# Optimization experiments

Measured on AMD Instinct MI355X. Metric: run time of the kernel, lower is better.

Reference implementation:

```python
import jax, jax.numpy as jnp
import numpy as np

B, R, NB, T = 32, 96, 5, 2048
FEAT_DIM = 64
SPARSITY = 0.2


def _per_band(X, community, W1, b1, W2, b2):
    # X: [R, T] wavelet coeffs for one (batch, band) slice
    n, t = X.shape
    f32 = X.dtype
    # --- functional connectivity (cosine of centered signals == Pearson corr) ---
    Xc = X - X.mean(axis=1, keepdims=True)
    norm = jnp.linalg.norm(Xc, axis=1, keepdims=True)
    norm = jnp.where(norm == 0, 1.0, norm)
    C = (Xc @ Xc.T) / (norm * norm.T)
    C = jnp.nan_to_num(C, nan=0.0)
    C = C * (1.0 - jnp.eye(n, dtype=f32))  # zero diagonal
    # --- quantile sparsification over strict lower triangle ---
    ti, tj = np.tril_indices(n, -1)
    thr = jnp.quantile(jnp.abs(C[ti, tj]), 1.0 - SPARSITY)
    A = C * (jnp.abs(C) >= thr).astype(f32)  # graph_type == 'weighted'
    # --- node features (5-dim, averaged over regions) ---
    mean_f = X.mean(axis=1)
    std_f = jnp.std(X, axis=1, ddof=1)  # torch.std is unbiased
    energy_f = (X ** 2).sum(axis=1)
    maxamp_f = jnp.abs(X).max(axis=1)
    ps = jnp.abs(jnp.fft.fft(X, axis=1)) ** 2
    ps = ps[:, : t // 2]
    s = ps.sum(axis=1, keepdims=True)
    s = jnp.where(s == 0, 1.0, s)
    p = ps / s
    ent_f = -(p * jnp.log(p + 1e-10)).sum(axis=1)
    node5 = jnp.stack([mean_f, std_f, energy_f, maxamp_f, ent_f], axis=1).mean(axis=0)
    # --- graph properties (6-dim) on binarized adjacency ---
    Bm = (A != 0).astype(f32)
    ne = Bm.sum() / 2.0
    density = ne / (n * (n - 1) / 2.0)
    deg = Bm.sum(axis=1)
    avg_deg = deg.mean()
    A2 = Bm @ Bm
    tri = (A2 * Bm).sum() / 6.0
    poss = (deg * (deg - 1.0)).sum() / 2.0
    clus = jnp.where(poss > 0, tri / jnp.where(poss > 0, poss, 1.0), 0.0)
    # global efficiency: safe reciprocal (zero where A+I == 0; original would emit inf)
    denom = Bm + jnp.eye(n, dtype=f32)
    eff = jnp.where(denom > 0, 1.0 / jnp.where(denom > 0, denom, 1.0), 0.0).sum() / (n * (n - 1))
    # approximate modularity with fixed 2-community assignment (deterministic)
    m2 = 2.0 * ne
    m2_safe = jnp.where(m2 > 0, m2, 1.0)
    same = (community[:, None] == community[None, :]) & (~jnp.eye(n, dtype=bool))
    expected = jnp.outer(deg, deg) / m2_safe
    mod = jnp.where(m2 > 0, (same * (Bm - expected)).sum() / m2_safe, 0.0)
    props = jnp.stack([ne, density, avg_deg, clus, eff, mod])
    feat11 = jnp.concatenate([node5, props])  # [11]
    # --- feature encoder MLP (dropout is identity at inference) ---
    h = jnp.maximum(feat11 @ W1.T + b1, 0.0)
    return A, h @ W2.T + b2


def _forward(wavelet_coeffs, frequency_bands, community, W1, b1, W2, b2):
    b, r, nb, t = wavelet_coeffs.shape
    Xs = wavelet_coeffs.transpose(0, 2, 1, 3).reshape(b * nb, r, t)  # [B*NB, R, T]
    A, F = jax.vmap(_per_band, in_axes=(0, None, None, None, None, None))(
        Xs, community, W1, b1, W2, b2)
    return A.reshape(b, nb, r, r), F.reshape(b, nb, -1)


def setup_inputs() -> dict:
    key = jax.random.key(0)
    k0, k1, k2, k3, k4 = jax.random.split(key, 5)
    wavelet_coeffs = jax.random.normal(k0, (B, R, NB, T), dtype=jnp.float32)
    frequency_bands = jax.random.uniform(k1, (NB, 2), dtype=jnp.float32)
    community = jax.random.randint(k2, (R,), 0, 2)
    W1 = jax.random.normal(k3, (32, 11), dtype=jnp.float32) * 0.3
    b1 = jnp.zeros((32,), jnp.float32)
    W2 = jax.random.normal(k4, (FEAT_DIM, 32), dtype=jnp.float32) * 0.18
    b2 = jnp.zeros((FEAT_DIM,), jnp.float32)
    return {"wavelet_coeffs": wavelet_coeffs, "frequency_bands": frequency_bands,
            "community": community, "W1": W1, "b1": b1, "W2": W2, "b2": b2}


def reference(wavelet_coeffs, frequency_bands, community, W1, b1, W2, b2):
    return _forward(wavelet_coeffs, frequency_bands, community, W1, b1, W2, b2)
```

## Files before the change

### kernel.cpp

```cpp
#include <hip/hip_runtime.h>
#include <hip/hip_bf16.h>
#include <math.h>
#include <float.h>

#ifndef M_PI
#define M_PI 3.14159265358979323846
#endif

#define NBANDS 160
#define RR 96
#define TT 2048
#define NTRIL 4560
#define A_ELEMS ((size_t)NBANDS * RR * RR)
#define NBIN 16384
#define MAXCAND 512

#define PHI(L) ((L) ^ (((L) >> 5) & 31))

typedef float  f32x4  __attribute__((ext_vector_type(4)));
typedef __bf16 bf16x8 __attribute__((ext_vector_type(8)));
typedef __bf16 bf16x4 __attribute__((ext_vector_type(4)));

__device__ inline double blockReduceSum(double v, double* sred) {
    for (int off = 32; off > 0; off >>= 1) v += __shfl_down(v, off, 64);
    int lane = threadIdx.x & 63, wid = threadIdx.x >> 6;
    if (lane == 0) sred[wid] = v;
    __syncthreads();
    int nw = (blockDim.x + 63) >> 6;
    if (threadIdx.x == 0) {
        double r = sred[0];
        for (int i = 1; i < nw; i++) r += sred[i];
        sred[0] = r;
    }
    __syncthreads();
    double r = sred[0];
    __syncthreads();
    return r;
}

__device__ inline void blockReduceSum4(double v0, double v1, double v2, double v3,
                                       double* sred, double out[4]) {
    for (int off = 32; off > 0; off >>= 1) {
        v0 += __shfl_down(v0, off, 64);
        v1 += __shfl_down(v1, off, 64);
        v2 += __shfl_down(v2, off, 64);
        v3 += __shfl_down(v3, off, 64);
    }
    int lane = threadIdx.x & 63, wid = threadIdx.x >> 6;
    if (lane == 0) {
        sred[wid * 4 + 0] = v0; sred[wid * 4 + 1] = v1;
        sred[wid * 4 + 2] = v2; sred[wid * 4 + 3] = v3;
    }
    __syncthreads();
    if (threadIdx.x < 4) {
        double r = sred[threadIdx.x] + sred[4 + threadIdx.x]
                 + sred[8 + threadIdx.x] + sred[12 + threadIdx.x];
        sred[16 + threadIdx.x] = r;
    }
    __syncthreads();
    out[0] = sred[16]; out[1] = sred[17]; out[2] = sred[18]; out[3] = sred[19];
    __syncthreads();
}

__device__ inline void blockReduceSum2(double v0, double v1,
                                       double* sred, double out[2]) {
    for (int off = 32; off > 0; off >>= 1) {
        v0 += __shfl_down(v0, off, 64);
        v1 += __shfl_down(v1, off, 64);
    }
    int lane = threadIdx.x & 63, wid = threadIdx.x >> 6;
    if (lane == 0) { sred[wid * 2 + 0] = v0; sred[wid * 2 + 1] = v1; }
    __syncthreads();
    if (threadIdx.x < 2) {
        double r = sred[threadIdx.x] + sred[2 + threadIdx.x]
                 + sred[4 + threadIdx.x] + sred[6 + threadIdx.x];
        sred[8 + threadIdx.x] = r;
    }
    __syncthreads();
    out[0] = sred[8]; out[1] = sred[9];
    __syncthreads();
}

__device__ inline void blockReduceMax2(double v0, double v1,
                                       double* sred, double out[2]) {
    for (int off = 32; off > 0; off >>= 1) {
        v0 = fmax(v0, __shfl_down(v0, off, 64));
        v1 = fmax(v1, __shfl_down(v1, off, 64));
    }
    int lane = threadIdx.x & 63, wid = threadIdx.x >> 6;
    if (lane == 0) { sred[wid * 2 + 0] = v0; sred[wid * 2 + 1] = v1; }
    __syncthreads();
    if (threadIdx.x < 2) {
        double r = fmax(fmax(sred[threadIdx.x], sred[2 + threadIdx.x]),
                        fmax(sred[4 + threadIdx.x], sred[6 + threadIdx.x]));
        sred[8 + threadIdx.x] = r;
    }
    __syncthreads();
    out[0] = sred[8]; out[1] = sred[9];
    __syncthreads();
}

__global__ void twiddle_kernel(float* tw) {
    int k = blockIdx.x * blockDim.x + threadIdx.x;
    if (k < 1024) {
        double ang = -2.0 * M_PI * (double)k / 2048.0;
        tw[2 * k]     = (float)cos(ang);
        tw[2 * k + 1] = (float)sin(ang);
    }
}

#define BFLY(r1, r2, WR, WI) do { \
    float _wr = (WR), _wi = (WI); \
    float _tr = _wr * yr[r2] - _wi * yi[r2]; \
    float _ti = _wr * yi[r2] + _wi * yr[r2]; \
    yr[r2] = yr[r1] - _tr; yi[r2] = yi[r1] - _ti; \
    yr[r1] += _tr; yi[r1] += _ti; } while (0)

__global__ __launch_bounds__(256) void rowstat_fft_kernel(
    const float* __restrict__ wc, const float* __restrict__ tw,
    double* __restrict__ rowstats)
{
    __shared__ float re[TT];
    __shared__ float im[TT];
    __shared__ double sred[24];
    __shared__ float bcast[4];

    int t = threadIdx.x;
    int g0 = blockIdx.x * 2;
    int g1 = g0 + 1;

    int band = g0 / RR, r0 = g0 % RR;
    int b = band / 5, nb = band % 5;
    size_t base0 = ((size_t)(b * RR + r0) * 5 + nb) * TT;
    size_t base1 = base0 + (size_t)5 * TT;

    float s0 = 0.f, s1 = 0.f, q0 = 0.f, q1 = 0.f, m0 = 0.f, m1 = 0.f;
#pragma unroll
    for (int c = 0; c < 8; c++) {
        int i = t + c * 256;
        float af = wc[base0 + i];
        float bf = wc[base1 + i];
        int P = PHI(i);
        re[P] = af; im[P] = bf;
        s0 += af; s1 += bf;
        q0 = fmaf(af, af, q0); q1 = fmaf(bf, bf, q1);
        m0 = fmaxf(m0, fabsf(af)); m1 = fmaxf(m1, fabsf(bf));
    }
    __syncthreads();

    double S4[4], M2[2];
    blockReduceSum4((double)s0, (double)s1, (double)q0, (double)q1, sred, S4);
    blockReduceMax2((double)m0, (double)m1, sred, M2);
    double SUM0 = S4[0], SUM1 = S4[1], SQ0 = S4[2], SQ1 = S4[3];
    double MX0 = M2[0], MX1 = M2[1];

    float yr[8], yi[8];

#pragma unroll
    for (int j = 0; j < 8; j++) {
        int p = 8 * t + j;
        int L = (int)(__brev((unsigned)p) >> 21);
        int P = PHI(L);
        yr[j] = re[P]; yi[j] = im[P];
    }

    const float RC = 0.70710678f;
    BFLY(0, 1, 1.0f, 0.0f); BFLY(2, 3, 1.0f, 0.0f);
    BFLY(4, 5, 1.0f, 0.0f); BFLY(6, 7, 1.0f, 0.0f);
    BFLY(0, 2, 1.0f, 0.0f); BFLY(1, 3, 0.0f, -1.0f);
    BFLY(4, 6, 1.0f, 0.0f); BFLY(5, 7, 0.0f, -1.0f);
    BFLY(0, 4, 1.0f, 0.0f); BFLY(1, 5, RC, -RC);
    BFLY(2, 6, 0.0f, -1.0f); BFLY(3, 7, -RC, -RC);

    __syncthreads();
#pragma unroll
    for (int j = 0; j < 8; j++) {
        int P = PHI(8 * t + j);
        re[P] = yr[j]; im[P] = yi[j];
    }
    __syncthreads();
    int oo = t & 7;
    int bb64 = 4 * ((t >> 3) & 7) + (t >> 6);
#pragma unroll
    for (int k = 0; k < 8; k++) {
        int P = PHI(64 * bb64 + 8 * k + oo);
        yr[k] = re[P]; yi[k] = im[P];
    }

    {
        int k0 = oo << 7;
        float w0r = tw[2 * k0], w0i = tw[2 * k0 + 1];
        BFLY(0, 1, w0r, w0i); BFLY(2, 3, w0r, w0i);
        BFLY(4, 5, w0r, w0i); BFLY(6, 7, w0r, w0i);
        int ka = oo << 6, kb = (oo + 8) << 6;
        float war = tw[2 * ka], wai = tw[2 * ka + 1];
        float wbr = tw[2 * kb], wbi = tw[2 * kb + 1];
        BFLY(0, 2, war, wai); BFLY(1, 3, wbr, wbi);
        BFLY(4, 6, war, wai); BFLY(5, 7, wbr, wbi);
        int kc0 = oo << 5, kc1 = (oo + 8) << 5, kc2 = (oo + 16) << 5, kc3 = (oo + 24) << 5;
        BFLY(0, 4, tw[2 * kc0], tw[2 * kc0 + 1]);
        BFLY(1, 5, tw[2 * kc1], tw[2 * kc1 + 1]);
        BFLY(2, 6, tw[2 * kc2], tw[2 * kc2 + 1]);
        BFLY(3, 7, tw[2 * kc3], tw[2 * kc3 + 1]);
    }

    __syncthreads();
#pragma unroll
    for (int k = 0; k < 8; k++) {
        int P = PHI(64 * bb64 + 8 * k + oo);
        re[P] = yr[k]; im[P] = yi[k];
    }
    __syncthreads();
    int O3 = t & 63, Wq = t >> 6;
#pragma unroll
    for (int s = 0; s < 2; s++) {
        int B3 = Wq + 4 * s;
#pragma unroll
        for (int k = 0; k < 4; k++) {
            int P = PHI(256 * B3 + 64 * k + O3);
            yr[4 * s + k] = re[P]; yi[4 * s + k] = im[P];
        }
    }

    {
        int kt = O3 << 4;
        float w0r = tw[2 * kt], w0i = tw[2 * kt + 1];
        int ka = O3 << 3, kb = (O3 + 64) << 3;
        float war = tw[2 * ka], wai = tw[2 * ka + 1];
        float wbr = tw[2 * kb], wbi = tw[2 * kb + 1];
        BFLY(0, 1, w0r, w0i); BFLY(2, 3, w0r, w0i);
        BFLY(4, 5, w0r, w0i); BFLY(6, 7, w0r, w0i);
        BFLY(0, 2, war, wai); BFLY(1, 3, wbr, wbi);
        BFLY(4, 6, war, wai); BFLY(5, 7, wbr, wbi);
    }

    __syncthreads();
#pragma unroll
    for (int s = 0; s < 2; s++) {
        int B3 = Wq + 4 * s;
#pragma unroll
        for (int k = 0; k < 4; k++) {
            int P = PHI(256 * B3 + 64 * k + O3);
            re[P] = yr[4 * s + k]; im[P] = yi[4 * s + k];
        }
    }
    __syncthreads();
#pragma unroll
    for (int k = 0; k < 8; k++) {
        int P = PHI(256 * k + t);
        yr[k] = re[P]; yi[k] = im[P];
    }

    {
        int k9 = t << 2;
        float w0r = tw[2 * k9], w0i = tw[2 * k9 + 1];
        BFLY(0, 1, w0r, w0i); BFLY(2, 3, w0r, w0i);
        BFLY(4, 5, w0r, w0i); BFLY(6, 7, w0r, w0i);
        int ka = t << 1, kb = (t + 256) << 1;
        float war = tw[2 * ka], wai = tw[2 * ka + 1];
        float wbr = tw[2 * kb], wbi = tw[2 * kb + 1];
        BFLY(0, 2, war, wai); BFLY(1, 3, wbr, wbi);
        BFLY(4, 6, war, wai); BFLY(5, 7, wbr, wbi);
        BFLY(0, 4, tw[2 * t], tw[2 * t + 1]);
        BFLY(1, 5, tw[2 * (t + 256)], tw[2 * (t + 256) + 1]);
        BFLY(2, 6, tw[2 * (t + 512)], tw[2 * (t + 512) + 1]);
        BFLY(3, 7, tw[2 * (t + 768)], tw[2 * (t + 768) + 1]);
    }

    __syncthreads();
#pragma unroll
    for (int k = 0; k < 8; k++) {
        int P = PHI(256 * k + t);
        re[P] = yr[k]; im[P] = yi[k];
    }
    __syncthreads();

    float psa[8], psb[8];
#pragma unroll
    for (int k = 0; k < 8; k++) {
        int q = (2048 - t - 256 * k) & 2047;
        int P = PHI(q);
        float prr = re[P], pii = im[P];
        float sr = yr[k] + prr, di = yi[k] - pii;
        float si = yi[k] + pii, dr = yr[k] - prr;
        psa[k] = 0.25f * (sr * sr + di * di);
        psb[k] = 0.25f * (si * si + dr * dr);
    }

    float la = 0.f, lb = 0.f;
#pragma unroll
    for (int k = 0; k < 8; k++) { la += psa[k]; lb += psb[k]; }
    double SS[2];
    blockReduceSum2((double)la, (double)lb, sred, SS);
    double SAall = SS[0], SBall = SS[1];
    if (t == 0) {
        bcast[0] = psa[0]; bcast[1] = psa[4];
        bcast[2] = psb[0]; bcast[3] = psb[4];
    }
    __syncthreads();
    double Sa = 0.5 * (SAall + (double)bcast[0] - (double)bcast[1]);
    double Sb = 0.5 * (SBall + (double)bcast[2] - (double)bcast[3]);
    if (Sa == 0.0) Sa = 1.0;
    if (Sb == 0.0) Sb = 1.0;
    float invSa = (float)(1.0 / Sa), invSb = (float)(1.0 / Sb);

    float ea = 0.f, eb = 0.f;
#pragma unroll
    for (int k = 0; k < 8; k++) {
        float pa = psa[k] * invSa;
        float pb = psb[k] * invSb;
        ea += pa * __logf(pa + 1e-10f);
        eb += pb * __logf(pb + 1e-10f);
    }
    double EE[2];
    blockReduceSum2((double)ea, (double)eb, sred, EE);
    double EAall = EE[0], EBall = EE[1];

    if (t == 0) {
        float pa0 = psa[0] * invSa, pa4 = psa[4] * invSa;
        float pb0 = psb[0] * invSb, pb4 = psb[4] * invSb;
        double TA = 0.5 * (EAall + (double)(pa0 * __logf(pa0 + 1e-10f))
                                 - (double)(pa4 * __logf(pa4 + 1e-10f)));
        double TB = 0.5 * (EBall + (double)(pb0 * __logf(pb0 + 1e-10f))
                                 - (double)(pb4 * __logf(pb4 + 1e-10f)));
        double mean0 = SUM0 / (double)TT;
        double mean1 = SUM1 / (double)TT;
        double nsq0 = SQ0 - (double)TT * mean0 * mean0; if (nsq0 < 0) nsq0 = 0;
        double nsq1 = SQ1 - (double)TT * mean1 * mean1; if (nsq1 < 0) nsq1 = 0;
        double* w0 = rowstats + (size_t)g0 * 6;
        double* w1 = rowstats + (size_t)g1 * 6;
        double n0 = sqrt(nsq0), n1 = sqrt(nsq1);
        w0[0] = mean0; w0[1] = (n0 == 0.0 ? 1.0 : n0); w0[2] = sqrt(nsq0 / 2047.0);
        w0[3] = SQ0;   w0[4] = MX0;                    w0[5] = -TA;
        w1[0] = mean1; w1[1] = (n1 == 0.0 ? 1.0 : n1); w1[2] = sqrt(nsq1 / 2047.0);
        w1[3] = SQ1;   w1[4] = MX1;                    w1[5] = -TB;
    }
}

__global__ void zero_kernel(float4* __restrict__ p, int n4) {
    int i = blockIdx.x * blockDim.x + threadIdx.x;
    if (i < n4) p[i] = make_float4(0.f, 0.f, 0.f, 0.f);
}

#define KS 8
#define CHUNK 256
#define BKS 64
#define GPITCH 72
template <bool USE_PART>
__global__ __launch_bounds__(384) void gram_mfma_kernel(
    const float* __restrict__ wc, float* __restrict__ G)
{
    __shared__ __attribute__((aligned(16))) __bf16 sh_hi[RR][GPITCH];
    __shared__ __attribute__((aligned(16))) __bf16 sh_lo[RR][GPITCH];

    int bid = blockIdx.x;
    int band = bid / KS, chunk = bid % KS;
    int b = band / 5, nb = band % 5;
    size_t bandbase = ((size_t)b * RR * 5 + nb) * TT + (size_t)chunk * CHUNK;

    int t = threadIdx.x;
    int wave = t >> 6, lane = t & 63;
    int m16 = lane & 15, quad = lane >> 4;
    int arow = wave * 16 + m16;

    f32x4 acc[6];
#pragma unroll
    for (int ct = 0; ct < 6; ct++) acc[ct] = (f32x4){0.f, 0.f, 0.f, 0.f};

    for (int stage = 0; stage < CHUNK / BKS; stage++) {
        int k0 = stage * BKS;
#pragma unroll
        for (int i = 0; i < 4; i++) {
            int gid = t + i * 384;
            int row = gid >> 4, c4 = gid & 15;
            float4 v = *(const float4*)(wc + bandbase + (size_t)row * (5 * TT) + k0 + c4 * 4);
            __bf16 h0 = (__bf16)v.x, h1 = (__bf16)v.y, h2 = (__bf16)v.z, h3 = (__bf16)v.w;
            __bf16 l0 = (__bf16)(v.x - (float)h0);
            __bf16 l1 = (__bf16)(v.y - (float)h1);
            __bf16 l2 = (__bf16)(v.z - (float)h2);
            __bf16 l3 = (__bf16)(v.w - (float)h3);
            *(bf16x4*)&sh_hi[row][c4 * 4] = (bf16x4){h0, h1, h2, h3};
            *(bf16x4*)&sh_lo[row][c4 * 4] = (bf16x4){l0, l1, l2, l3};
        }
        __syncthreads();
#pragma unroll
        for (int ks = 0; ks < BKS / 32; ks++) {
            int ko = ks * 32 + quad * 8;
            bf16x8 ah = *(const bf16x8*)&sh_hi[arow][ko];
            bf16x8 al = *(const bf16x8*)&sh_lo[arow][ko];
#pragma unroll
            for (int ct = 0; ct < 6; ct++) {
                int brow = ct * 16 + m16;
                bf16x8 bh = *(const bf16x8*)&sh_hi[brow][ko];
                bf16x8 bl = *(const bf16x8*)&sh_lo[brow][ko];
                acc[ct] = __builtin_amdgcn_mfma_f32_16x16x32_bf16(ah, bh, acc[ct], 0, 0, 0);
                acc[ct] = __builtin_amdgcn_mfma_f32_16x16x32_bf16(ah, bl, acc[ct], 0, 0, 0);
                acc[ct] = __builtin_amdgcn_mfma_f32_16x16x32_bf16(al, bh, acc[ct], 0, 0, 0);
            }
        }
        __syncthreads();
    }

    if (USE_PART) {
        float* Gp = G + (size_t)bid * (RR * RR);
#pragma unroll
        for (int ct = 0; ct < 6; ct++) {
#pragma unroll
            for (int r = 0; r < 4; r++) {
                int grow = wave * 16 + quad * 4 + r;
                int gcol = ct * 16 + m16;
                Gp[grow * RR + gcol] = acc[ct][r];
            }
        }
    } else {
        float* Gb = G + (size_t)band * (RR * RR);
#pragma unroll
        for (int ct = 0; ct < 6; ct++) {
#pragma unroll
            for (int r = 0; r < 4; r++) {
                int grow = wave * 16 + quad * 4 + r;
                int gcol = ct * 16 + m16;
                atomicAdd(&Gb[grow * RR + gcol], acc[ct][r]);
            }
        }
    }
}

template <bool USE_PART>
__global__ __launch_bounds__(256) void normalize_kernel(
    float* __restrict__ G, const float* __restrict__ Gpart,
    const double* __restrict__ rowstats)
{
    int e = blockIdx.x * 256 + threadIdx.x;
    if (e >= (int)(NBANDS * RR * RR)) return;
    int band = e / (RR * RR);
    int rem = e % (RR * RR);
    int i = rem / RR, j = rem % RR;
    double g;
    if (USE_PART) {
        const float* p = Gpart + (size_t)band * KS * (RR * RR) + rem;
        float acc = 0.f;
#pragma unroll
        for (int c = 0; c < KS; c++) acc += p[(size_t)c * (RR * RR)];
        g = (double)acc;
    } else {
        g = (double)G[e];
    }
    const double* rsi = rowstats + (size_t)(band * RR + i) * 6;
    const double* rsj = rowstats + (size_t)(band * RR + j) * 6;
    double c = (g - (double)TT * rsi[0] * rsj[0]) / (rsi[1] * rsj[1]);
    if (i == j) c = 0.0;
    G[e] = (float)c;
}

__global__ __launch_bounds__(256) void quantile_kernel(
    const float* __restrict__ C, double* __restrict__ thr)
{
    __shared__ int hist[NBIN];
    __shared__ int chunk[256];
    __shared__ float cand[MAXCAND];
    __shared__ int ctrl[4];

    int band = blockIdx.x, t = threadIdx.x;
    const float* Cb = C + (size_t)band * (RR * RR);

    for (int i = t; i < NBIN; i += 256) hist[i] = 0;
    if (t == 0) ctrl[3] = 0;
    __syncthreads();

    for (int idx = t; idx < RR * RR; idx += 256) {
        int i = idx / RR, j = idx % RR;
        if (j < i) {
            float val = fabsf(Cb[idx]);
            int bin = (int)(val * (float)NBIN);
            bin = bin > (NBIN - 1) ? (NBIN - 1) : bin;
            atomicAdd(&hist[bin], 1);
        }
    }
    __syncthreads();

    int cs = 0;
    for (int i = 0; i < 64; i++) cs += hist[t * 64 + i];
    chunk[t] = cs;
    __syncthreads();

    if (t == 0) {
        int r0 = 3647, r1 = 3648;
        int cum = 0, c0 = 0;
        while (c0 < 256 && cum + chunk[c0] <= r0) { cum += chunk[c0]; c0++; }
        int bin = c0 * 64, cb = cum;
        while (cb + hist[bin] <= r0) { cb += hist[bin]; bin++; }
        int B0 = bin, cumB0 = cb;
        int bin1 = bin, cb1 = cb;
        while (cb1 + hist[bin1] <= r1) { cb1 += hist[bin1]; bin1++; }
        ctrl[0] = B0; ctrl[1] = bin1; ctrl[2] = cumB0;
    }
    __syncthreads();

    int B0 = ctrl[0], B1 = ctrl[1];
    for (int idx = t; idx < RR * RR; idx += 256) {
        int i = idx / RR, j = idx % RR;
        if (j < i) {
            float val = fabsf(Cb[idx]);
            int bin = (int)(val * (float)NBIN);
            bin = bin > (NBIN - 1) ? (NBIN - 1) : bin;
            if (bin >= B0 && bin <= B1) {
                int k = atomicAdd(&ctrl[3], 1);
                if (k < MAXCAND) cand[k] = val;
            }
        }
    }
    __syncthreads();

    if (t == 0) {
        int n = ctrl[3]; if (n > MAXCAND) n = MAXCAND;
        for (int i = 1; i < n; i++) {
            float key = cand[i]; int j = i - 1;
            while (j >= 0 && cand[j] > key) { cand[j + 1] = cand[j]; j--; }
            cand[j + 1] = key;
        }
        int r0 = 3647 - ctrl[2];
        int r1 = 3648 - ctrl[2];
        double v0 = (double)cand[r0], v1 = (double)cand[r1];
        thr[band] = v0 + 0.2 * (v1 - v0);
    }
}

__global__ __launch_bounds__(256) void graph_feat_kernel(
    const double* __restrict__ thrA,
    const double* __restrict__ rowstats, const int* __restrict__ community,
    const float* __restrict__ W1, const float* __restrict__ b1,
    const float* __restrict__ W2, const float* __restrict__ b2,
    float* __restrict__ A_out, float* __restrict__ F_out)
{
    __shared__ unsigned char Bm[RR][RR];
    __shared__ unsigned long long msk[RR][2];
    __shared__ int deg[RR];
    __shared__ double sred[8];
    __shared__ double feat[11];
    __shared__ double h[32];

    int band = blockIdx.x, t = threadIdx.x;
    double thr = thrA[band];
    float* Ab = A_out + (size_t)band * (RR * RR);

    for (int idx = t; idx < RR * RR; idx += 256) {
        float c = Ab[idx];
        bool keep = ((double)fabsf(c) >= thr);
        Bm[idx / RR][idx % RR] = (keep && c != 0.0f) ? 1 : 0;
        Ab[idx] = keep ? c : 0.0f;
    }
    __syncthreads();

    if (t < RR) {
        unsigned long long m0 = 0, m1 = 0; int d = 0;
        for (int j = 0; j < RR; j++) {
            if (Bm[t][j]) { d++; if (j < 64) m0 |= (1ull << j); else m1 |= (1ull << (j - 64)); }
        }
        msk[t][0] = m0; msk[t][1] = m1; deg[t] = d;
    }
    __syncthreads();

    double triord = 0, ein = 0, expin = 0;
    for (int idx = t; idx < RR * RR; idx += 256) {
        int i = idx / RR, j = idx % RR;
        if (Bm[i][j])
            triord += (double)(__popcll(msk[i][0] & msk[j][0]) +
                               __popcll(msk[i][1] & msk[j][1]));
        if (i != j && community[i] == community[j]) {
            ein += (double)Bm[i][j];
            expin += (double)deg[i] * (double)deg[j];
        }
    }
    double TRI   = blockReduceSum(triord, sred);
    double EIN   = blockReduceSum(ein, sred);
    double EXPIN = blockReduceSum(expin, sred);
    double dv = (t < RR) ? (double)deg[t] : 0.0;
    double DEGS = blockReduceSum(dv, sred);
    double POSS2 = blockReduceSum((t < RR) ? dv * (dv - 1.0) : 0.0, sred);

    const double* rs = rowstats + (size_t)band * RR * 6;
    double N0 = blockReduceSum((t < RR) ? rs[t * 6 + 0] : 0.0, sred);
    double N1 = blockReduceSum((t < RR) ? rs[t * 6 + 2] : 0.0, sred);
    double N2 = blockReduceSum((t < RR) ? rs[t * 6 + 3] : 0.0, sred);
    double N3 = blockReduceSum((t < RR) ? rs[t * 6 + 4] : 0.0, sred);
    double N4 = blockReduceSum((t < RR) ? rs[t * 6 + 5] : 0.0, sred);

    if (t == 0) {
        double ne = 0.5 * DEGS;
        feat[0] = N0 / (double)RR;
        feat[1] = N1 / (double)RR;
        feat[2] = N2 / (double)RR;
        feat[3] = N3 / (double)RR;
        feat[4] = N4 / (double)RR;
        feat[5] = ne;
        feat[6] = ne / (double)NTRIL;
        feat[7] = DEGS / (double)RR;
        double tri = TRI / 6.0, poss = POSS2 * 0.5;
        feat[8] = (poss > 0.0) ? tri / poss : 0.0;
        feat[9] = ((double)RR + DEGS) / ((double)RR * (double)(RR - 1));
        double m2 = DEGS;
        feat[10] = (m2 > 0.0) ? (EIN - EXPIN / m2) / m2 : 0.0;
    }
    __syncthreads();

    if (t < 32) {
        double a = (double)b1[t];
        for (int k = 0; k < 11; k++) a += (double)W1[t * 11 + k] * feat[k];
        h[t] = (a > 0.0) ? a : 0.0;
    }
    __syncthreads();
    if (t < 64) {
        double a = (double)b2[t];
        for (int j = 0; j < 32; j++) a += (double)W2[t * 32 + j] * h[j];
        F_out[(size_t)band * 64 + t] = (float)a;
    }
}

extern "C" void kernel_launch(void* const* d_in, const int* in_sizes, int n_in,
                              void* d_out, int out_size, void* d_ws, size_t ws_size,
                              hipStream_t stream) {
    const float* wc        = (const float*)d_in[0];
    const int*   community = (const int*)d_in[2];
    const float* W1        = (const float*)d_in[3];
    const float* b1        = (const float*)d_in[4];
    const float* W2        = (const float*)d_in[5];
    const float* b2        = (const float*)d_in[6];

    float* A_out = (float*)d_out;
    float* F_out = A_out + A_ELEMS;

    char* ws = (char*)d_ws;
    float*  tw       = (float*)ws;
    double* rowstats = (double*)(ws + 8192);
    double* thr      = (double*)(ws + 745472);
    const size_t PART_OFF   = 747520;
    const size_t PART_BYTES = (size_t)NBANDS * KS * RR * RR * sizeof(float);
    float* Gpart = (float*)(ws + PART_OFF);
    bool use_part = (ws_size >= PART_OFF + PART_BYTES);

    hipLaunchKernelGGL(twiddle_kernel, dim3(4), dim3(256), 0, stream, tw);
    hipLaunchKernelGGL(rowstat_fft_kernel, dim3(NBANDS * RR / 2), dim3(256), 0, stream,
                       wc, tw, rowstats);
    if (use_part) {
        hipLaunchKernelGGL(HIP_KERNEL_NAME(gram_mfma_kernel<true>),
                           dim3(NBANDS * KS), dim3(384), 0, stream, wc, Gpart);
        hipLaunchKernelGGL(HIP_KERNEL_NAME(normalize_kernel<true>),
                           dim3((int)((NBANDS * RR * RR + 255) / 256)), dim3(256), 0, stream,
                           A_out, Gpart, rowstats);
    } else {
        int n4 = (int)(A_ELEMS / 4);
        hipLaunchKernelGGL(zero_kernel, dim3((n4 + 255) / 256), dim3(256), 0, stream,
                           (float4*)A_out, n4);
        hipLaunchKernelGGL(HIP_KERNEL_NAME(gram_mfma_kernel<false>),
                           dim3(NBANDS * KS), dim3(384), 0, stream, wc, A_out);
        hipLaunchKernelGGL(HIP_KERNEL_NAME(normalize_kernel<false>),
                           dim3((int)((NBANDS * RR * RR + 255) / 256)), dim3(256), 0, stream,
                           A_out, A_out, rowstats);
    }
    hipLaunchKernelGGL(quantile_kernel, dim3(NBANDS), dim3(256), 0, stream, A_out, thr);
    hipLaunchKernelGGL(graph_feat_kernel, dim3(NBANDS), dim3(256), 0, stream,
                       thr, rowstats, community, W1, b1, W2, b2, A_out, F_out);
}
```

Before: 323.0 us.

## Fuse gram, normalize, quantile and graph features into one per-band kernel

Replaces the split-K gram kernel plus the normalize, quantile and graph-feature kernels with one kernel per band. That kernel computes the full 2048-long gram product with register prefetch, normalizes into shared memory, builds the histogram, finds the quantile threshold, and derives masks with wave ballots. This removes the partial-sum and correlation-matrix round trips through global memory and several launches. The trade-off is that parallelism for the gram product drops from 1280 blocks to 160, each looping over the whole time axis with heavy shared memory use. Twiddle loads are also vectorized as float2, and the histogram shrinks to 8192 bins.

```diff
diff --git a/kernel.cpp b/kernel.cpp
--- a/kernel.cpp
+++ b/kernel.cpp
@@ -12,31 +12,17 @@
 #define TT 2048
 #define NTRIL 4560
 #define A_ELEMS ((size_t)NBANDS * RR * RR)
-#define NBIN 16384
+#define NBIN 8192
 #define MAXCAND 512
+#define BKS 64
+#define GPITCH 72
+#define FBLK 384
 
 #define PHI(L) ((L) ^ (((L) >> 5) & 31))
 
 typedef float  f32x4  __attribute__((ext_vector_type(4)));
 typedef __bf16 bf16x8 __attribute__((ext_vector_type(8)));
 typedef __bf16 bf16x4 __attribute__((ext_vector_type(4)));
-
-__device__ inline double blockReduceSum(double v, double* sred) {
-    for (int off = 32; off > 0; off >>= 1) v += __shfl_down(v, off, 64);
-    int lane = threadIdx.x & 63, wid = threadIdx.x >> 6;
-    if (lane == 0) sred[wid] = v;
-    __syncthreads();
-    int nw = (blockDim.x + 63) >> 6;
-    if (threadIdx.x == 0) {
-        double r = sred[0];
-        for (int i = 1; i < nw; i++) r += sred[i];
-        sred[0] = r;
-    }
-    __syncthreads();
-    double r = sred[0];
-    __syncthreads();
-    return r;
-}
 
 __device__ inline void blockReduceSum4(double v0, double v1, double v2, double v3,
                                        double* sred, double out[4]) {
@@ -47,18 +33,20 @@
         v3 += __shfl_down(v3, off, 64);
     }
     int lane = threadIdx.x & 63, wid = threadIdx.x >> 6;
+    int nw = blockDim.x >> 6;
     if (lane == 0) {
         sred[wid * 4 + 0] = v0; sred[wid * 4 + 1] = v1;
         sred[wid * 4 + 2] = v2; sred[wid * 4 + 3] = v3;
     }
     __syncthreads();
     if (threadIdx.x < 4) {
-        double r = sred[threadIdx.x] + sred[4 + threadIdx.x]
-                 + sred[8 + threadIdx.x] + sred[12 + threadIdx.x];
-        sred[16 + threadIdx.x] = r;
-    }
-    __syncthreads();
-    out[0] = sred[16]; out[1] = sred[17]; out[2] = sred[18]; out[3] = sred[19];
+        double r = sred[threadIdx.x];
+        for (int w = 1; w < nw; w++) r += sred[w * 4 + threadIdx.x];
+        sred[nw * 4 + threadIdx.x] = r;
+    }
+    __syncthreads();
+    out[0] = sred[nw * 4 + 0]; out[1] = sred[nw * 4 + 1];
+    out[2] = sred[nw * 4 + 2]; out[3] = sred[nw * 4 + 3];
     __syncthreads();
 }
 
@@ -69,15 +57,16 @@
         v1 += __shfl_down(v1, off, 64);
     }
     int lane = threadIdx.x & 63, wid = threadIdx.x >> 6;
+    int nw = blockDim.x >> 6;
     if (lane == 0) { sred[wid * 2 + 0] = v0; sred[wid * 2 + 1] = v1; }
     __syncthreads();
     if (threadIdx.x < 2) {
-        double r = sred[threadIdx.x] + sred[2 + threadIdx.x]
-                 + sred[4 + threadIdx.x] + sred[6 + threadIdx.x];
-        sred[8 + threadIdx.x] = r;
-    }
-    __syncthreads();
-    out[0] = sred[8]; out[1] = sred[9];
+        double r = sred[threadIdx.x];
+        for (int w = 1; w < nw; w++) r += sred[w * 2 + threadIdx.x];
+        sred[nw * 2 + threadIdx.x] = r;
+    }
+    __syncthreads();
+    out[0] = sred[nw * 2 + 0]; out[1] = sred[nw * 2 + 1];
     __syncthreads();
 }
 
@@ -88,15 +77,16 @@
         v1 = fmax(v1, __shfl_down(v1, off, 64));
     }
     int lane = threadIdx.x & 63, wid = threadIdx.x >> 6;
+    int nw = blockDim.x >> 6;
     if (lane == 0) { sred[wid * 2 + 0] = v0; sred[wid * 2 + 1] = v1; }
     __syncthreads();
     if (threadIdx.x < 2) {
-        double r = fmax(fmax(sred[threadIdx.x], sred[2 + threadIdx.x]),
-                        fmax(sred[4 + threadIdx.x], sred[6 + threadIdx.x]));
-        sred[8 + threadIdx.x] = r;
-    }
-    __syncthreads();
-    out[0] = sred[8]; out[1] = sred[9];
+        double r = sred[threadIdx.x];
+        for (int w = 1; w < nw; w++) r = fmax(r, sred[w * 2 + threadIdx.x]);
+        sred[nw * 2 + threadIdx.x] = r;
+    }
+    __syncthreads();
+    out[0] = sred[nw * 2 + 0]; out[1] = sred[nw * 2 + 1];
     __syncthreads();
 }
 
@@ -122,7 +112,7 @@
 {
     __shared__ float re[TT];
     __shared__ float im[TT];
-    __shared__ double sred[24];
+    __shared__ double sred[32];
     __shared__ float bcast[4];
 
     int t = threadIdx.x;
@@ -133,6 +123,7 @@
     int b = band / 5, nb = band % 5;
     size_t base0 = ((size_t)(b * RR + r0) * 5 + nb) * TT;
     size_t base1 = base0 + (size_t)5 * TT;
+    const float2* twv = (const float2*)tw;
 
     float s0 = 0.f, s1 = 0.f, q0 = 0.f, q1 = 0.f, m0 = 0.f, m1 = 0.f;
 #pragma unroll
@@ -188,20 +179,19 @@
     }
 
     {
-        int k0 = oo << 7;
-        float w0r = tw[2 * k0], w0i = tw[2 * k0 + 1];
-        BFLY(0, 1, w0r, w0i); BFLY(2, 3, w0r, w0i);
-        BFLY(4, 5, w0r, w0i); BFLY(6, 7, w0r, w0i);
-        int ka = oo << 6, kb = (oo + 8) << 6;
-        float war = tw[2 * ka], wai = tw[2 * ka + 1];
-        float wbr = tw[2 * kb], wbi = tw[2 * kb + 1];
-        BFLY(0, 2, war, wai); BFLY(1, 3, wbr, wbi);
-        BFLY(4, 6, war, wai); BFLY(5, 7, wbr, wbi);
-        int kc0 = oo << 5, kc1 = (oo + 8) << 5, kc2 = (oo + 16) << 5, kc3 = (oo + 24) << 5;
-        BFLY(0, 4, tw[2 * kc0], tw[2 * kc0 + 1]);
-        BFLY(1, 5, tw[2 * kc1], tw[2 * kc1 + 1]);
-        BFLY(2, 6, tw[2 * kc2], tw[2 * kc2 + 1]);
-        BFLY(3, 7, tw[2 * kc3], tw[2 * kc3 + 1]);
+        float2 w0 = twv[oo << 7];
+        BFLY(0, 1, w0.x, w0.y); BFLY(2, 3, w0.x, w0.y);
+        BFLY(4, 5, w0.x, w0.y); BFLY(6, 7, w0.x, w0.y);
+        float2 wa = twv[oo << 6];
+        float2 wb = twv[(oo + 8) << 6];
+        BFLY(0, 2, wa.x, wa.y); BFLY(1, 3, wb.x, wb.y);
+        BFLY(4, 6, wa.x, wa.y); BFLY(5, 7, wb.x, wb.y);
+        float2 wc0 = twv[oo << 5], wc1 = twv[(oo + 8) << 5];
+        float2 wc2 = twv[(oo + 16) << 5], wc3 = twv[(oo + 24) << 5];
+        BFLY(0, 4, wc0.x, wc0.y);
+        BFLY(1, 5, wc1.x, wc1.y);
+        BFLY(2, 6, wc2.x, wc2.y);
+        BFLY(3, 7, wc3.x, wc3.y);
     }
 
     __syncthreads();
@@ -223,15 +213,13 @@
     }
 
     {
-        int kt = O3 << 4;
-        float w0r = tw[2 * kt], w0i = tw[2 * kt + 1];
-        int ka = O3 << 3, kb = (O3 + 64) << 3;
-        float war = tw[2 * ka], wai = tw[2 * ka + 1];
-        float wbr = tw[2 * kb], wbi = tw[2 * kb + 1];
-        BFLY(0, 1, w0r, w0i); BFLY(2, 3, w0r, w0i);
-        BFLY(4, 5, w0r, w0i); BFLY(6, 7, w0r, w0i);
-        BFLY(0, 2, war, wai); BFLY(1, 3, wbr, wbi);
-        BFLY(4, 6, war, wai); BFLY(5, 7, wbr, wbi);
+        float2 w0 = twv[O3 << 4];
+        float2 wa = twv[O3 << 3];
+        float2 wb = twv[(O3 + 64) << 3];
+        BFLY(0, 1, w0.x, w0.y); BFLY(2, 3, w0.x, w0.y);
+        BFLY(4, 5, w0.x, w0.y); BFLY(6, 7, w0.x, w0.y);
+        BFLY(0, 2, wa.x, wa.y); BFLY(1, 3, wb.x, wb.y);
+        BFLY(4, 6, wa.x, wa.y); BFLY(5, 7, wb.x, wb.y);
     }
 
     __syncthreads();
@@ -252,19 +240,19 @@
     }
 
     {
-        int k9 = t << 2;
-        float w0r = tw[2 * k9], w0i = tw[2 * k9 + 1];
-        BFLY(0, 1, w0r, w0i); BFLY(2, 3, w0r, w0i);
-        BFLY(4, 5, w0r, w0i); BFLY(6, 7, w0r, w0i);
-        int ka = t << 1, kb = (t + 256) << 1;
-        float war = tw[2 * ka], wai = tw[2 * ka + 1];
-        float wbr = tw[2 * kb], wbi = tw[2 * kb + 1];
-        BFLY(0, 2, war, wai); BFLY(1, 3, wbr, wbi);
-        BFLY(4, 6, war, wai); BFLY(5, 7, wbr, wbi);
-        BFLY(0, 4, tw[2 * t], tw[2 * t + 1]);
-        BFLY(1, 5, tw[2 * (t + 256)], tw[2 * (t + 256) + 1]);
-        BFLY(2, 6, tw[2 * (t + 512)], tw[2 * (t + 512) + 1]);
-        BFLY(3, 7, tw[2 * (t + 768)], tw[2 * (t + 768) + 1]);
+        float2 w0 = twv[t << 2];
+        float2 wa = twv[t << 1];
+        float2 wb = twv[(t + 256) << 1];
+        BFLY(0, 1, w0.x, w0.y); BFLY(2, 3, w0.x, w0.y);
+        BFLY(4, 5, w0.x, w0.y); BFLY(6, 7, w0.x, w0.y);
+        BFLY(0, 2, wa.x, wa.y); BFLY(1, 3, wb.x, wb.y);
+        BFLY(4, 6, wa.x, wa.y); BFLY(5, 7, wb.x, wb.y);
+        float2 wf0 = twv[t], wf1 = twv[t + 256];
+        float2 wf2 = twv[t + 512], wf3 = twv[t + 768];
+        BFLY(0, 4, wf0.x, wf0.y);
+        BFLY(1, 5, wf1.x, wf1.y);
+        BFLY(2, 6, wf2.x, wf2.y);
+        BFLY(3, 7, wf3.x, wf3.y);
     }
 
     __syncthreads();
@@ -337,52 +325,83 @@
     }
 }
 
-__global__ void zero_kernel(float4* __restrict__ p, int n4) {
-    int i = blockIdx.x * blockDim.x + threadIdx.x;
-    if (i < n4) p[i] = make_float4(0.f, 0.f, 0.f, 0.f);
-}
-
-#define KS 8
-#define CHUNK 256
-#define BKS 64
-#define GPITCH 72
-template <bool USE_PART>
-__global__ __launch_bounds__(384) void gram_mfma_kernel(
-    const float* __restrict__ wc, float* __restrict__ G)
+#define CVW(v, row, c4) do { \
+    __bf16 _h0 = (__bf16)v.x, _h1 = (__bf16)v.y, _h2 = (__bf16)v.z, _h3 = (__bf16)v.w; \
+    __bf16 _l0 = (__bf16)(v.x - (float)_h0), _l1 = (__bf16)(v.y - (float)_h1); \
+    __bf16 _l2 = (__bf16)(v.z - (float)_h2), _l3 = (__bf16)(v.w - (float)_h3); \
+    *(bf16x4*)&sh_hi[row][(c4) * 4] = (bf16x4){_h0, _h1, _h2, _h3}; \
+    *(bf16x4*)&sh_lo[row][(c4) * 4] = (bf16x4){_l0, _l1, _l2, _l3}; } while (0)
+
+__global__ __launch_bounds__(FBLK) void fused_gram_finalize_kernel(
+    const float* __restrict__ wc, const double* __restrict__ rowstats,
+    const int* __restrict__ community,
+    const float* __restrict__ W1, const float* __restrict__ b1,
+    const float* __restrict__ W2, const float* __restrict__ b2,
+    float* __restrict__ A_out, float* __restrict__ F_out)
 {
     __shared__ __attribute__((aligned(16))) __bf16 sh_hi[RR][GPITCH];
     __shared__ __attribute__((aligned(16))) __bf16 sh_lo[RR][GPITCH];
-
-    int bid = blockIdx.x;
-    int band = bid / KS, chunk = bid % KS;
+    __shared__ float Cs[RR][RR];
+    __shared__ int hist[NBIN];
+    __shared__ int chunkv[256];
+    __shared__ float cand[MAXCAND];
+    __shared__ int ctrl[4];
+    __shared__ double mean_s[RR], inv_s[RR];
+    __shared__ int comm_s[RR];
+    __shared__ unsigned long long msk[RR][2];
+    __shared__ int deg[RR];
+    __shared__ double sred[32];
+    __shared__ double feat[11];
+    __shared__ double hmlp[32];
+    __shared__ double thr_s;
+
+    int band = blockIdx.x, t = threadIdx.x;
     int b = band / 5, nb = band % 5;
-    size_t bandbase = ((size_t)b * RR * 5 + nb) * TT + (size_t)chunk * CHUNK;
-
-    int t = threadIdx.x;
+    size_t bandbase = ((size_t)b * RR * 5 + nb) * TT;
+    const double* rsb = rowstats + (size_t)band * RR * 6;
+
+    if (t < RR) {
+        mean_s[t] = rsb[t * 6 + 0];
+        inv_s[t]  = 1.0 / rsb[t * 6 + 1];
+        comm_s[t] = community[t];
+    }
+    for (int i = t; i < NBIN; i += FBLK) hist[i] = 0;
+    if (t == 0) ctrl[3] = 0;
+
     int wave = t >> 6, lane = t & 63;
     int m16 = lane & 15, quad = lane >> 4;
     int arow = wave * 16 + m16;
 
+    int gid0 = t, gid1 = t + 384, gid2 = t + 768, gid3 = t + 1152;
+    int row0 = gid0 >> 4, c40 = gid0 & 15;
+    int row1 = gid1 >> 4, c41 = gid1 & 15;
+    int row2 = gid2 >> 4, c42 = gid2 & 15;
+    int row3 = gid3 >> 4, c43 = gid3 & 15;
+    const float* p0 = wc + bandbase + (size_t)row0 * (5 * TT) + c40 * 4;
+    const float* p1 = wc + bandbase + (size_t)row1 * (5 * TT) + c41 * 4;
+    const float* p2 = wc + bandbase + (size_t)row2 * (5 * TT) + c42 * 4;
+    const float* p3 = wc + bandbase + (size_t)row3 * (5 * TT) + c43 * 4;
+
     f32x4 acc[6];
 #pragma unroll
     for (int ct = 0; ct < 6; ct++) acc[ct] = (f32x4){0.f, 0.f, 0.f, 0.f};
 
-    for (int stage = 0; stage < CHUNK / BKS; stage++) {
-        int k0 = stage * BKS;
-#pragma unroll
-        for (int i = 0; i < 4; i++) {
-            int gid = t + i * 384;
-            int row = gid >> 4, c4 = gid & 15;
-            float4 v = *(const float4*)(wc + bandbase + (size_t)row * (5 * TT) + k0 + c4 * 4);
-            __bf16 h0 = (__bf16)v.x, h1 = (__bf16)v.y, h2 = (__bf16)v.z, h3 = (__bf16)v.w;
-            __bf16 l0 = (__bf16)(v.x - (float)h0);
-            __bf16 l1 = (__bf16)(v.y - (float)h1);
-            __bf16 l2 = (__bf16)(v.z - (float)h2);
-            __bf16 l3 = (__bf16)(v.w - (float)h3);
-            *(bf16x4*)&sh_hi[row][c4 * 4] = (bf16x4){h0, h1, h2, h3};
-            *(bf16x4*)&sh_lo[row][c4 * 4] = (bf16x4){l0, l1, l2, l3};
-        }
+    float4 pr0 = *(const float4*)(p0);
+    float4 pr1 = *(const float4*)(p1);
+    float4 pr2 = *(const float4*)(p2);
+    float4 pr3 = *(const float4*)(p3);
+
+    for (int st = 0; st < TT / BKS; st++) {
+        CVW(pr0, row0, c40); CVW(pr1, row1, c41);
+        CVW(pr2, row2, c42); CVW(pr3, row3, c43);
         __syncthreads();
+        if (st + 1 < TT / BKS) {
+            int k0 = (st + 1) * BKS;
+            pr0 = *(const float4*)(p0 + k0);
+            pr1 = *(const float4*)(p1 + k0);
+            pr2 = *(const float4*)(p2 + k0);
+            pr3 = *(const float4*)(p3 + k0);
+        }
 #pragma unroll
         for (int ks = 0; ks < BKS / 32; ks++) {
             int ko = ks * 32 + quad * 8;
@@ -401,94 +420,40 @@
         __syncthreads();
     }
 
-    if (USE_PART) {
-        float* Gp = G + (size_t)bid * (RR * RR);
-#pragma unroll
-        for (int ct = 0; ct < 6; ct++) {
-#pragma unroll
-            for (int r = 0; r < 4; r++) {
-                int grow = wave * 16 + quad * 4 + r;
-                int gcol = ct * 16 + m16;
-                Gp[grow * RR + gcol] = acc[ct][r];
+#pragma unroll
+    for (int ct = 0; ct < 6; ct++) {
+#pragma unroll
+        for (int r = 0; r < 4; r++) {
+            int grow = wave * 16 + quad * 4 + r;
+            int gcol = ct * 16 + m16;
+            double cd = ((double)acc[ct][r]
+                         - (double)TT * mean_s[grow] * mean_s[gcol])
+                        * (inv_s[grow] * inv_s[gcol]);
+            if (grow == gcol) cd = 0.0;
+            float cf = (float)cd;
+            Cs[grow][gcol] = cf;
+            if (gcol < grow) {
+                float val = fabsf(cf);
+                int bin = (int)(val * (float)NBIN);
+                bin = bin > (NBIN - 1) ? (NBIN - 1) : bin;
+                atomicAdd(&hist[bin], 1);
             }
         }
-    } else {
-        float* Gb = G + (size_t)band * (RR * RR);
-#pragma unroll
-        for (int ct = 0; ct < 6; ct++) {
-#pragma unroll
-            for (int r = 0; r < 4; r++) {
-                int grow = wave * 16 + quad * 4 + r;
-                int gcol = ct * 16 + m16;
-                atomicAdd(&Gb[grow * RR + gcol], acc[ct][r]);
-            }
-        }
-    }
-}
-
-template <bool USE_PART>
-__global__ __launch_bounds__(256) void normalize_kernel(
-    float* __restrict__ G, const float* __restrict__ Gpart,
-    const double* __restrict__ rowstats)
-{
-    int e = blockIdx.x * 256 + threadIdx.x;
-    if (e >= (int)(NBANDS * RR * RR)) return;
-    int band = e / (RR * RR);
-    int rem = e % (RR * RR);
-    int i = rem / RR, j = rem % RR;
-    double g;
-    if (USE_PART) {
-        const float* p = Gpart + (size_t)band * KS * (RR * RR) + rem;
-        float acc = 0.f;
-#pragma unroll
-        for (int c = 0; c < KS; c++) acc += p[(size_t)c * (RR * RR)];
-        g = (double)acc;
-    } else {
-        g = (double)G[e];
-    }
-    const double* rsi = rowstats + (size_t)(band * RR + i) * 6;
-    const double* rsj = rowstats + (size_t)(band * RR + j) * 6;
-    double c = (g - (double)TT * rsi[0] * rsj[0]) / (rsi[1] * rsj[1]);
-    if (i == j) c = 0.0;
-    G[e] = (float)c;
-}
-
-__global__ __launch_bounds__(256) void quantile_kernel(
-    const float* __restrict__ C, double* __restrict__ thr)
-{
-    __shared__ int hist[NBIN];
-    __shared__ int chunk[256];
-    __shared__ float cand[MAXCAND];
-    __shared__ int ctrl[4];
-
-    int band = blockIdx.x, t = threadIdx.x;
-    const float* Cb = C + (size_t)band * (RR * RR);
-
-    for (int i = t; i < NBIN; i += 256) hist[i] = 0;
-    if (t == 0) ctrl[3] = 0;
-    __syncthreads();
-
-    for (int idx = t; idx < RR * RR; idx += 256) {
-        int i = idx / RR, j = idx % RR;
-        if (j < i) {
-            float val = fabsf(Cb[idx]);
-            int bin = (int)(val * (float)NBIN);
-            bin = bin > (NBIN - 1) ? (NBIN - 1) : bin;
-            atomicAdd(&hist[bin], 1);
-        }
-    }
-    __syncthreads();
-
-    int cs = 0;
-    for (int i = 0; i < 64; i++) cs += hist[t * 64 + i];
-    chunk[t] = cs;
+    }
+    __syncthreads();
+
+    if (t < 256) {
+        int cs = 0;
+        for (int i = 0; i < NBIN / 256; i++) cs += hist[t * (NBIN / 256) + i];
+        chunkv[t] = cs;
+    }
     __syncthreads();
 
     if (t == 0) {
         int r0 = 3647, r1 = 3648;
         int cum = 0, c0 = 0;
-        while (c0 < 256 && cum + chunk[c0] <= r0) { cum += chunk[c0]; c0++; }
-        int bin = c0 * 64, cb = cum;
+        while (c0 < 256 && cum + chunkv[c0] <= r0) { cum += chunkv[c0]; c0++; }
+        int bin = c0 * (NBIN / 256), cb = cum;
         while (cb + hist[bin] <= r0) { cb += hist[bin]; bin++; }
         int B0 = bin, cumB0 = cb;
         int bin1 = bin, cb1 = cb;
@@ -498,10 +463,10 @@
     __syncthreads();
 
     int B0 = ctrl[0], B1 = ctrl[1];
-    for (int idx = t; idx < RR * RR; idx += 256) {
+    for (int idx = t; idx < RR * RR; idx += FBLK) {
         int i = idx / RR, j = idx % RR;
         if (j < i) {
-            float val = fabsf(Cb[idx]);
+            float val = fabsf(Cs[i][j]);
             int bin = (int)(val * (float)NBIN);
             bin = bin > (NBIN - 1) ? (NBIN - 1) : bin;
             if (bin >= B0 && bin <= B1) {
@@ -522,69 +487,57 @@
         int r0 = 3647 - ctrl[2];
         int r1 = 3648 - ctrl[2];
         double v0 = (double)cand[r0], v1 = (double)cand[r1];
-        thr[band] = v0 + 0.2 * (v1 - v0);
-    }
-}
-
-__global__ __launch_bounds__(256) void graph_feat_kernel(
-    const double* __restrict__ thrA,
-    const double* __restrict__ rowstats, const int* __restrict__ community,
-    const float* __restrict__ W1, const float* __restrict__ b1,
-    const float* __restrict__ W2, const float* __restrict__ b2,
-    float* __restrict__ A_out, float* __restrict__ F_out)
-{
-    __shared__ unsigned char Bm[RR][RR];
-    __shared__ unsigned long long msk[RR][2];
-    __shared__ int deg[RR];
-    __shared__ double sred[8];
-    __shared__ double feat[11];
-    __shared__ double h[32];
-
-    int band = blockIdx.x, t = threadIdx.x;
-    double thr = thrA[band];
+        thr_s = v0 + 0.2 * (v1 - v0);
+    }
+    __syncthreads();
+    double thr = thr_s;
+
     float* Ab = A_out + (size_t)band * (RR * RR);
-
-    for (int idx = t; idx < RR * RR; idx += 256) {
-        float c = Ab[idx];
-        bool keep = ((double)fabsf(c) >= thr);
-        Bm[idx / RR][idx % RR] = (keep && c != 0.0f) ? 1 : 0;
-        Ab[idx] = keep ? c : 0.0f;
-    }
-    __syncthreads();
-
-    if (t < RR) {
-        unsigned long long m0 = 0, m1 = 0; int d = 0;
-        for (int j = 0; j < RR; j++) {
-            if (Bm[t][j]) { d++; if (j < 64) m0 |= (1ull << j); else m1 |= (1ull << (j - 64)); }
-        }
-        msk[t][0] = m0; msk[t][1] = m1; deg[t] = d;
+    for (int idx = t; idx < RR * RR; idx += FBLK) {
+        float cf = Cs[idx / RR][idx % RR];
+        bool keep = ((double)fabsf(cf) >= thr);
+        Ab[idx] = keep ? cf : 0.f;
+    }
+
+    for (int i = wave; i < RR; i += 6) {
+        float vlo = Cs[i][lane];
+        bool klo = ((double)fabsf(vlo) >= thr) && (vlo != 0.f);
+        unsigned long long blo = __ballot(klo);
+        float vhi = Cs[i][64 + (lane & 31)];
+        bool khi = (lane < 32) && ((double)fabsf(vhi) >= thr) && (vhi != 0.f);
+        unsigned long long bhi = __ballot(khi) & 0xffffffffull;
+        if (lane == 0) {
+            msk[i][0] = blo; msk[i][1] = bhi;
+            deg[i] = __popcll(blo) + __popcll(bhi);
+        }
     }
     __syncthreads();
 
     double triord = 0, ein = 0, expin = 0;
-    for (int idx = t; idx < RR * RR; idx += 256) {
+    for (int idx = t; idx < RR * RR; idx += FBLK) {
         int i = idx / RR, j = idx % RR;
-        if (Bm[i][j])
-            triord += (double)(__popcll(msk[i][0] & msk[j][0]) +
-                               __popcll(msk[i][1] & msk[j][1]));
-        if (i != j && community[i] == community[j]) {
-            ein += (double)Bm[i][j];
+        unsigned long long mi0 = msk[i][0], mi1 = msk[i][1];
+        bool bij = (((j < 64) ? (mi0 >> j) : (mi1 >> (j - 64))) & 1ull) != 0;
+        if (bij)
+            triord += (double)(__popcll(mi0 & msk[j][0]) +
+                               __popcll(mi1 & msk[j][1]));
+        if (i != j && comm_s[i] == comm_s[j]) {
+            ein += bij ? 1.0 : 0.0;
             expin += (double)deg[i] * (double)deg[j];
         }
     }
-    double TRI   = blockReduceSum(triord, sred);
-    double EIN   = blockReduceSum(ein, sred);
-    double EXPIN = blockReduceSum(expin, sred);
     double dv = (t < RR) ? (double)deg[t] : 0.0;
-    double DEGS = blockReduceSum(dv, sred);
-    double POSS2 = blockReduceSum((t < RR) ? dv * (dv - 1.0) : 0.0, sred);
-
-    const double* rs = rowstats + (size_t)band * RR * 6;
-    double N0 = blockReduceSum((t < RR) ? rs[t * 6 + 0] : 0.0, sred);
-    double N1 = blockReduceSum((t < RR) ? rs[t * 6 + 2] : 0.0, sred);
-    double N2 = blockReduceSum((t < RR) ? rs[t * 6 + 3] : 0.0, sred);
-    double N3 = blockReduceSum((t < RR) ? rs[t * 6 + 4] : 0.0, sred);
-    double N4 = blockReduceSum((t < RR) ? rs[t * 6 + 5] : 0.0, sred);
+    double R1[4], R2[4], R3[2];
+    blockReduceSum4(triord, ein, expin, dv, sred, R1);
+    blockReduceSum4((t < RR) ? dv * (dv - 1.0) : 0.0,
+                    (t < RR) ? rsb[t * 6 + 0] : 0.0,
+                    (t < RR) ? rsb[t * 6 + 2] : 0.0,
+                    (t < RR) ? rsb[t * 6 + 3] : 0.0, sred, R2);
+    blockReduceSum2((t < RR) ? rsb[t * 6 + 4] : 0.0,
+                    (t < RR) ? rsb[t * 6 + 5] : 0.0, sred, R3);
+    double TRI = R1[0], EIN = R1[1], EXPIN = R1[2], DEGS = R1[3];
+    double POSS2 = R2[0], N0 = R2[1], N1 = R2[2], N2 = R2[3];
+    double N3 = R3[0], N4 = R3[1];
 
     if (t == 0) {
         double ne = 0.5 * DEGS;
@@ -607,12 +560,12 @@
     if (t < 32) {
         double a = (double)b1[t];
         for (int k = 0; k < 11; k++) a += (double)W1[t * 11 + k] * feat[k];
-        h[t] = (a > 0.0) ? a : 0.0;
+        hmlp[t] = (a > 0.0) ? a : 0.0;
     }
     __syncthreads();
     if (t < 64) {
         double a = (double)b2[t];
-        for (int j = 0; j < 32; j++) a += (double)W2[t * 32 + j] * h[j];
+        for (int j = 0; j < 32; j++) a += (double)W2[t * 32 + j] * hmlp[j];
         F_out[(size_t)band * 64 + t] = (float)a;
     }
 }
@@ -633,32 +586,10 @@
     char* ws = (char*)d_ws;
     float*  tw       = (float*)ws;
     double* rowstats = (double*)(ws + 8192);
-    double* thr      = (double*)(ws + 745472);
-    const size_t PART_OFF   = 747520;
-    const size_t PART_BYTES = (size_t)NBANDS * KS * RR * RR * sizeof(float);
-    float* Gpart = (float*)(ws + PART_OFF);
-    bool use_part = (ws_size >= PART_OFF + PART_BYTES);
 
     hipLaunchKernelGGL(twiddle_kernel, dim3(4), dim3(256), 0, stream, tw);
     hipLaunchKernelGGL(rowstat_fft_kernel, dim3(NBANDS * RR / 2), dim3(256), 0, stream,
                        wc, tw, rowstats);
-    if (use_part) {
-        hipLaunchKernelGGL(HIP_KERNEL_NAME(gram_mfma_kernel<true>),
-                           dim3(NBANDS * KS), dim3(384), 0, stream, wc, Gpart);
-        hipLaunchKernelGGL(HIP_KERNEL_NAME(normalize_kernel<true>),
-                           dim3((int)((NBANDS * RR * RR + 255) / 256)), dim3(256), 0, stream,
-                           A_out, Gpart, rowstats);
-    } else {
-        int n4 = (int)(A_ELEMS / 4);
-        hipLaunchKernelGGL(zero_kernel, dim3((n4 + 255) / 256), dim3(256), 0, stream,
-                           (float4*)A_out, n4);
-        hipLaunchKernelGGL(HIP_KERNEL_NAME(gram_mfma_kernel<false>),
-                           dim3(NBANDS * KS), dim3(384), 0, stream, wc, A_out);
-        hipLaunchKernelGGL(HIP_KERNEL_NAME(normalize_kernel<false>),
-                           dim3((int)((NBANDS * RR * RR + 255) / 256)), dim3(256), 0, stream,
-                           A_out, A_out, rowstats);
-    }
-    hipLaunchKernelGGL(quantile_kernel, dim3(NBANDS), dim3(256), 0, stream, A_out, thr);
-    hipLaunchKernelGGL(graph_feat_kernel, dim3(NBANDS), dim3(256), 0, stream,
-                       thr, rowstats, community, W1, b1, W2, b2, A_out, F_out);
-}
+    hipLaunchKernelGGL(fused_gram_finalize_kernel, dim3(NBANDS), dim3(FBLK), 0, stream,
+                       wc, rowstats, community, W1, b1, W2, b2, A_out, F_out);
+}
```

Result: faster. 304.2 us (-5.8%).
